# Optimization experiments

Measured on AMD Instinct MI355X. Metric: run time of the kernel, lower is better.

## Reference

```python
import jax, jax.numpy as jnp
import numpy as np

D_MODEL = 1024
NUM_HEADS = 16

def _dense_params(key, d_in, d_out):
    kw, _ = jax.random.split(key)
    # flax default: lecun_normal kernel, zeros bias
    W = jax.random.normal(kw, (d_in, d_out), dtype=jnp.float32) / np.sqrt(d_in)
    b = jnp.zeros((d_out,), dtype=jnp.float32)
    return W, b

def setup_inputs() -> dict:
    key = jax.random.key(0)
    ks = jax.random.split(key, 8)
    B, Tx, Tc = 2, 2048, 2048
    x = jax.random.normal(ks[0], (B, Tx, D_MODEL), dtype=jnp.float32)
    context = jax.random.normal(ks[1], (B, Tc, D_MODEL), dtype=jnp.float32)
    Wq, bq = _dense_params(ks[2], D_MODEL, D_MODEL)
    Wks, bks = _dense_params(ks[3], D_MODEL, D_MODEL)
    Wvs, bvs = _dense_params(ks[4], D_MODEL, D_MODEL)
    Wkc, bkc = _dense_params(ks[5], D_MODEL, D_MODEL)
    Wvc, bvc = _dense_params(ks[6], D_MODEL, D_MODEL)
    Wo, bo = _dense_params(ks[7], D_MODEL, D_MODEL)
    return {"x": x, "context": context,
            "Wq": Wq, "bq": bq, "Wks": Wks, "bks": bks, "Wvs": Wvs, "bvs": bvs,
            "Wkc": Wkc, "bkc": bkc, "Wvc": Wvc, "bvc": bvc, "Wo": Wo, "bo": bo}

def _split_heads(t, H):
    B, T, C = t.shape
    return t.reshape(B, T, H, C // H).transpose(0, 2, 1, 3)  # [B,H,T,hd]

def reference(x, context, Wq, bq, Wks, bks, Wvs, bvs, Wkc, bkc, Wvc, bvc, Wo, bo):
    H = NUM_HEADS
    head_dim = D_MODEL // H
    q = x @ Wq + bq
    k = jnp.concatenate([x @ Wks + bks, context @ Wkc + bkc], axis=1)
    v = jnp.concatenate([x @ Wvs + bvs, context @ Wvc + bvc], axis=1)
    q = _split_heads(q, H)  # [B,H,Tq,hd]
    k = _split_heads(k, H)  # [B,H,Tk,hd]
    v = _split_heads(v, H)
    attn = jnp.einsum('bhqd,bhkd->bhqk', q, k) / jnp.sqrt(jnp.float32(head_dim))
    attn = jax.nn.softmax(attn, axis=-1)
    out = jnp.einsum('bhqk,bhkd->bhqd', attn, v)
    B, _, Tq, _ = out.shape
    out = out.transpose(0, 2, 1, 3).reshape(B, Tq, D_MODEL)
    return out @ Wo + bo
```

## Files before the change

kernel.cpp:

```cpp
#include <hip/hip_runtime.h>
#include <hip/hip_bf16.h>
#include <math.h>


typedef _Float16 f16;
typedef _Float16 f16x8 __attribute__((ext_vector_type(8)));
typedef _Float16 f16x4v __attribute__((ext_vector_type(4)));
typedef _Float16 f16x2 __attribute__((ext_vector_type(2)));
typedef float    f32x4 __attribute__((ext_vector_type(4)));
typedef float    f32x16 __attribute__((ext_vector_type(16)));
typedef unsigned u32x4v __attribute__((ext_vector_type(4)));

#define MFMA_F16(a, b, c)  __builtin_amdgcn_mfma_f32_16x16x32_f16((a), (b), (c), 0, 0, 0)
#define MFMA32_F16(a, b, c) __builtin_amdgcn_mfma_f32_32x32x16_f16((a), (b), (c), 0, 0, 0)

#define QSCALE 0.18033688011112042f

__device__ __forceinline__ void glds16(const f16* g, f16* l) {
    __builtin_amdgcn_global_load_lds(
        (const __attribute__((address_space(1))) void*)g,
        (__attribute__((address_space(3))) void*)l, 16, 0, 0);
}

__device__ __forceinline__ unsigned pk16(float a, float b) {
    f16x2 t = { (f16)a, (f16)b };
    return __builtin_bit_cast(unsigned, t);
}

__global__ __launch_bounds__(256) void prep(
    const float4* __restrict__ x, const float4* __restrict__ ctx,
    f16x4v* __restrict__ xb, f16x4v* __restrict__ cb,
    const float* __restrict__ W0, const float* __restrict__ W1,
    const float* __restrict__ W2, const float* __restrict__ W3,
    const float* __restrict__ W4, const float* __restrict__ W5,
    f16* __restrict__ wt)
{
    if (blockIdx.x < 8192) {
        const int n4 = (2 * 2048 * 1024) / 4;
        int i = blockIdx.x * 256 + threadIdx.x;
        float4 v;
        f16x4v* dst;
        if (i < n4) { v = x[i];        dst = xb + i; }
        else        { v = ctx[i - n4]; dst = cb + (i - n4); }
        f16x4v h = { (f16)v.x, (f16)v.y, (f16)v.z, (f16)v.w };
        *dst = h;
        return;
    }
    const int idx = blockIdx.x - 8192;
    const int z = idx >> 10, rem = idx & 1023;
    const float* Ws[6] = { W0, W1, W2, W3, W4, W5 };
    const float* W = Ws[z];
    f16* Wt = wt + (size_t)z * (1024 * 1024);

    __shared__ float tile[32][33];
    const int tx = threadIdx.x & 31, ty = threadIdx.x >> 5;
    const int n0 = (rem & 31) * 32, k0 = (rem >> 5) * 32;

#pragma unroll
    for (int i = 0; i < 4; ++i) {
        int r = i * 8 + ty;
        tile[r][tx] = W[(size_t)(k0 + r) * 1024 + n0 + tx];
    }
    __syncthreads();
#pragma unroll
    for (int i = 0; i < 4; ++i) {
        int r = i * 8 + ty;
        Wt[(size_t)(n0 + r) * 1024 + k0 + tx] = (f16)tile[tx][r];
    }
}

#define GEMM_PROLOGUE(BN)                                                     \
    const int m0 = blockIdx.x * 128, n0 = blockIdx.y * (BN);                  \
    const int tid = threadIdx.x;                                              \
    const int w = tid >> 6, lane = tid & 63, quad = lane >> 4, l15 = lane & 15;\
    const int wm = (w >> 1) * 64, wn = (w & 1) * ((BN) / 2);                  \
    const int qsw = (quad ^ ((l15 >> 1) & 3)) * 8;                            \
    int gA[2], gB[(BN) / 64];                                                 \
    _Pragma("unroll")                                                         \
    for (int p = 0; p < 2; ++p) {                                             \
        int s = tid + p * 256;                                                \
        int r = (s >> 2) & 127, c = (s & 3) ^ ((s >> 3) & 3);                 \
        gA[p] = (m0 + r) * 1024 + c * 8;                                      \
    }                                                                         \
    _Pragma("unroll")                                                         \
    for (int p = 0; p < (BN) / 64; ++p) {                                     \
        int s = tid + p * 256;                                                \
        int r = (s >> 2) & ((BN) - 1), c = (s & 3) ^ ((s >> 3) & 3);          \
        gB[p] = (n0 + r) * 1024 + c * 8;                                      \
    }

#define GEMM_STAGE_TO(BN, buf, koff)                                          \
    _Pragma("unroll")                                                         \
    for (int p = 0; p < 2; ++p)                                               \
        glds16(&A[gA[p] + (koff)], &As[buf][(p * 256 + w * 64) * 8]);         \
    _Pragma("unroll")                                                         \
    for (int p = 0; p < (BN) / 64; ++p)                                       \
        glds16(&Bt[gB[p] + (koff)], &Bs[buf][(p * 256 + w * 64) * 8]);

__global__ __launch_bounds__(256) void proj_gemm(
    const f16* __restrict__ xb, const f16* __restrict__ cb,
    const f16* __restrict__ wt,
    const float* __restrict__ bq, const float* __restrict__ bks,
    const float* __restrict__ bkc, const float* __restrict__ bvs,
    const float* __restrict__ bvc,
    f16* __restrict__ qbuf, f16* __restrict__ kbuf, f16* __restrict__ vbuf)
{
    __shared__ alignas(16) f16 As[3][128 * 32];
    __shared__ alignas(16) f16 Bs[3][128 * 32];

    const int z = blockIdx.z;
    const f16* A = (z == 0 || z == 1 || z == 3) ? xb : cb;
    const int wslot = (z == 0) ? 0 : (z == 1) ? 1 : (z == 2) ? 3 : (z == 3) ? 2 : 4;
    const f16* Bt = wt + (size_t)wslot * 1048576;
    const float* bias = (z == 0) ? bq : (z == 1) ? bks : (z == 2) ? bkc
                        : (z == 3) ? bvs : bvc;
    const int roff = (z == 2 || z == 4) ? 2048 : 0;

    GEMM_PROLOGUE(128)
    f32x4 acc[4][4] = {};

    GEMM_STAGE_TO(128, 0, 0)
    GEMM_STAGE_TO(128, 1, 32)

    for (int it = 0; it < 32; ++it) {
        if (it < 31) { asm volatile("s_waitcnt vmcnt(4)" ::: "memory"); }
        else         { asm volatile("s_waitcnt vmcnt(0)" ::: "memory"); }
        __builtin_amdgcn_s_barrier();
        if (it + 2 < 32) {
            GEMM_STAGE_TO(128, (it + 2) % 3, (it + 2) * 32)
        }
        const f16* Asc = As[it % 3];
        const f16* Bsc = Bs[it % 3];
        f16x8 a[4], b[4];
#pragma unroll
        for (int i = 0; i < 4; ++i)
            a[i] = *(const f16x8*)&Asc[(wm + i * 16 + l15) * 32 + qsw];
#pragma unroll
        for (int i = 0; i < 4; ++i)
            b[i] = *(const f16x8*)&Bsc[(wn + i * 16 + l15) * 32 + qsw];
#pragma unroll
        for (int mi = 0; mi < 4; ++mi)
#pragma unroll
            for (int ni = 0; ni < 4; ++ni)
                acc[mi][ni] = MFMA_F16(a[mi], b[ni], acc[mi][ni]);
    }

#pragma unroll
    for (int mi = 0; mi < 4; ++mi) {
#pragma unroll
        for (int r = 0; r < 4; ++r) {
            int row = m0 + wm + mi * 16 + quad * 4 + r;
            int b_ = row >> 11, tok = row & 2047;
#pragma unroll
            for (int ni = 0; ni < 4; ++ni) {
                int col = n0 + wn + ni * 16 + l15;
                float v = acc[mi][ni][r] + bias[col];
                int bh = b_ * 16 + (col >> 6);
                int tg = roff + tok;
                if (z == 0) {
                    qbuf[((size_t)bh * 2048 + tok) * 64 + (col & 63)] = (f16)(v * QSCALE);
                } else if (z <= 2) {
                    kbuf[(size_t)bh * 262144 + (size_t)(tg >> 6) * 4096
                         + (size_t)((col >> 5) & 1) * 2048 + (tg & 63) * 32 + (col & 31)] = (f16)v;
                } else {
                    vbuf[(size_t)bh * 262144 + (size_t)tg * 64 + (col & 63)] = (f16)v;
                }
            }
        }
    }
}

__global__ __launch_bounds__(256) void transpose_v(
    const f16* __restrict__ vbuf, f16* __restrict__ vt)
{
    const int t = threadIdx.x;
    const int mt = t >> 3, md = t & 7;
    const int tok0 = blockIdx.x * 256 + mt * 8;
    const int z = blockIdx.y;
    f16x8 in[8];
#pragma unroll
    for (int i = 0; i < 8; ++i)
        in[i] = *(const f16x8*)&vbuf[((size_t)z * 4096 + tok0 + i) * 64 + md * 8];
    f16x8 ov[8];
#pragma unroll
    for (int j = 0; j < 8; ++j)
#pragma unroll
        for (int i = 0; i < 8; ++i) ov[j][i] = in[i][j];
    const int kt = tok0 >> 6, kks = (tok0 >> 5) & 1, kko = tok0 & 31;
#pragma unroll
    for (int j = 0; j < 8; ++j)
        *(f16x8*)&vt[(size_t)z * 262144 + (size_t)kt * 4096 + kks * 2048
                     + (md * 8 + j) * 32 + kko] = ov[j];
}

__global__ __launch_bounds__(256, 4) void attn_kernel(
    const f16* __restrict__ q, const f16* __restrict__ kb,
    const f16* __restrict__ vtb, f16* __restrict__ osplit,
    float* __restrict__ lsplit)
{
    __shared__ alignas(16) f16 K_lds[2][4096];
    __shared__ alignas(16) f16 V_lds[2][4096];

    const int tid = threadIdx.x;
    const int w = tid >> 6, lane = tid & 63;
    const int l31 = lane & 31, h = lane >> 5;
    const int bh = blockIdx.x, qt = blockIdx.y, sp = blockIdx.z;
    const int qbase = qt * 128;

    f16x8 qa[4];
    {
        const size_t qrow = ((size_t)bh * 2048 + qbase + w * 32 + l31) * 64;
#pragma unroll
        for (int kc = 0; kc < 4; ++kc)
            qa[kc] = *(const f16x8*)&q[qrow + kc * 16 + h * 8];
    }

    f32x16 o_acc[2] = {};
    float l_part = 0.f;

    const f16* ktile = kb + (size_t)bh * 262144 + (size_t)sp * 131072;
    const f16* vtile = vtb + (size_t)bh * 262144 + (size_t)sp * 131072;

    const int sco = ((tid >> 2) * 4 + ((tid & 3) ^ ((tid >> 3) & 3))) * 8;
    const int ksw = (l31 >> 1) & 3;
    const int wslot = w * 512;

    glds16(ktile + sco,        &K_lds[0][wslot]);
    glds16(ktile + 2048 + sco, &K_lds[0][2048 + wslot]);
    glds16(vtile + sco,        &V_lds[0][wslot]);
    glds16(vtile + 2048 + sco, &V_lds[0][2048 + wslot]);

    for (int kt = 0; kt < 32; ++kt) {
        const int cur = kt & 1;
        const f16* Kc = K_lds[cur];
        const f16* Vc = V_lds[cur];

        __syncthreads();

        if (kt != 31) {
            ktile += 4096; vtile += 4096;
            glds16(ktile + sco,        &K_lds[cur ^ 1][wslot]);
            glds16(ktile + 2048 + sco, &K_lds[cur ^ 1][2048 + wslot]);
            glds16(vtile + sco,        &V_lds[cur ^ 1][wslot]);
            glds16(vtile + 2048 + sco, &V_lds[cur ^ 1][2048 + wslot]);
        }

#pragma unroll
        for (int mt = 0; mt < 2; ++mt) {
            f32x16 s = {};
            __builtin_amdgcn_s_setprio(1);
#pragma unroll
            for (int kc = 0; kc < 4; ++kc) {
                f16x8 ka = *(const f16x8*)&Kc[(kc >> 1) * 2048
                             + (mt * 32 + l31) * 32
                             + ((((kc & 1) * 2 + h) ^ ksw)) * 8];
                s = MFMA32_F16(ka, qa[kc], s);
            }
            __builtin_amdgcn_s_setprio(0);

            float pe[16];
#pragma unroll
            for (int i = 0; i < 16; ++i) pe[i] = __builtin_amdgcn_exp2f(s[i]);

            {
                float t0 = (pe[0] + pe[1]) + (pe[2] + pe[3]);
                float t1 = (pe[4] + pe[5]) + (pe[6] + pe[7]);
                float t2 = (pe[8] + pe[9]) + (pe[10] + pe[11]);
                float t3 = (pe[12] + pe[13]) + (pe[14] + pe[15]);
                l_part += (t0 + t1) + (t2 + t3);
            }

#pragma unroll
            for (int c = 0; c < 2; ++c) {
                const int cb = c * 8;
                unsigned X0 = pk16(pe[cb + 0], pe[cb + 1]);
                unsigned X1 = pk16(pe[cb + 2], pe[cb + 3]);
                unsigned Y0 = pk16(pe[cb + 4], pe[cb + 5]);
                unsigned Y1 = pk16(pe[cb + 6], pe[cb + 7]);
                auto r0 = __builtin_amdgcn_permlane32_swap(X0, Y0, false, false);
                auto r1 = __builtin_amdgcn_permlane32_swap(X1, Y1, false, false);
                u32x4v pw;
                pw[0] = r0[0]; pw[1] = r1[0]; pw[2] = r0[1]; pw[3] = r1[1];
                f16x8 pfrag = __builtin_bit_cast(f16x8, pw);

                const int kchunk = mt * 2 + c;
                __builtin_amdgcn_s_setprio(1);
#pragma unroll
                for (int db = 0; db < 2; ++db) {
                    f16x8 va = *(const f16x8*)&Vc[(kchunk >> 1) * 2048
                                 + (db * 32 + l31) * 32
                                 + (((((kchunk & 1) * 2 + h)) ^ ksw)) * 8];
                    o_acc[db] = MFMA32_F16(va, pfrag, o_acc[db]);
                }
                __builtin_amdgcn_s_setprio(0);
            }
        }
    }

    float lf = l_part + __shfl_xor(l_part, 32, 64);
    float inv = 1.0f / lf;
    const int row = w * 32 + l31;
    const size_t sb = (size_t)(sp * 32 + bh) * 2048 + qbase;
    if (h == 0) lsplit[sb + row] = lf;
    const size_t obase = (sb + row) * 64;
#pragma unroll
    for (int db = 0; db < 2; ++db) {
#pragma unroll
        for (int g = 0; g < 4; ++g) {
            f16x4v ov;
#pragma unroll
            for (int i = 0; i < 4; ++i)
                ov[i] = (f16)(o_acc[db][g * 4 + i] * inv);
            *(f16x4v*)&osplit[obase + db * 32 + g * 8 + h * 4] = ov;
        }
    }
}

__global__ __launch_bounds__(256) void combine(
    const f16* __restrict__ osplit, const float* __restrict__ lsplit,
    f16* __restrict__ abuf)
{
    int idx = blockIdx.x * 256 + threadIdx.x;
    int d8 = idx & 7;
    int row = (idx >> 3) & 2047;
    int bh = idx >> 14;
    int b = bh >> 4, h = bh & 15;
    size_t base1 = ((size_t)bh * 2048 + row) * 64 + d8 * 8;
    size_t base2 = ((size_t)(32 + bh) * 2048 + row) * 64 + d8 * 8;
    float l1 = lsplit[bh * 2048 + row];
    float l2 = lsplit[65536 + bh * 2048 + row];
    float inv = 1.0f / (l1 + l2);
    float w1 = l1 * inv, w2 = l2 * inv;
    f16x8 a = *(const f16x8*)&osplit[base1];
    f16x8 c = *(const f16x8*)&osplit[base2];
    f16x8 out;
#pragma unroll
    for (int j = 0; j < 8; ++j)
        out[j] = (f16)(w1 * (float)a[j] + w2 * (float)c[j]);
    *(f16x8*)&abuf[((size_t)(b * 2048 + row)) * 1024 + h * 64 + d8 * 8] = out;
}

__global__ __launch_bounds__(256) void out_gemm(
    const f16* __restrict__ abuf, const f16* __restrict__ wt5,
    const float* __restrict__ bo, float* __restrict__ out)
{
    __shared__ alignas(16) f16 As[3][128 * 32];
    __shared__ alignas(16) f16 Bs[3][64 * 32];

    const f16* A = abuf;
    const f16* Bt = wt5;

    GEMM_PROLOGUE(64)
    f32x4 acc[4][2] = {};

    GEMM_STAGE_TO(64, 0, 0)
    GEMM_STAGE_TO(64, 1, 32)

    for (int it = 0; it < 32; ++it) {
        if (it < 31) { asm volatile("s_waitcnt vmcnt(3)" ::: "memory"); }
        else         { asm volatile("s_waitcnt vmcnt(0)" ::: "memory"); }
        __builtin_amdgcn_s_barrier();
        if (it + 2 < 32) {
            GEMM_STAGE_TO(64, (it + 2) % 3, (it + 2) * 32)
        }
        const f16* Asc = As[it % 3];
        const f16* Bsc = Bs[it % 3];
        f16x8 a[4], b[2];
#pragma unroll
        for (int i = 0; i < 4; ++i)
            a[i] = *(const f16x8*)&Asc[(wm + i * 16 + l15) * 32 + qsw];
#pragma unroll
        for (int i = 0; i < 2; ++i)
            b[i] = *(const f16x8*)&Bsc[(wn + i * 16 + l15) * 32 + qsw];
#pragma unroll
        for (int mi = 0; mi < 4; ++mi)
#pragma unroll
            for (int ni = 0; ni < 2; ++ni)
                acc[mi][ni] = MFMA_F16(a[mi], b[ni], acc[mi][ni]);
    }

#pragma unroll
    for (int mi = 0; mi < 4; ++mi) {
#pragma unroll
        for (int r = 0; r < 4; ++r) {
            int row = m0 + wm + mi * 16 + quad * 4 + r;
#pragma unroll
            for (int ni = 0; ni < 2; ++ni) {
                int col = n0 + wn + ni * 16 + l15;
                out[(size_t)row * 1024 + col] = acc[mi][ni][r] + bo[col];
            }
        }
    }
}

extern "C" void kernel_launch(void* const* d_in, const int* in_sizes, int n_in,
                              void* d_out, int out_size, void* d_ws, size_t ws_size,
                              hipStream_t stream)
{
    (void)in_sizes; (void)n_in; (void)out_size; (void)ws_size;

    const float* x    = (const float*)d_in[0];
    const float* ctx  = (const float*)d_in[1];
    const float* Wq   = (const float*)d_in[2];  const float* bq  = (const float*)d_in[3];
    const float* Wks  = (const float*)d_in[4];  const float* bks = (const float*)d_in[5];
    const float* Wvs  = (const float*)d_in[6];  const float* bvs = (const float*)d_in[7];
    const float* Wkc  = (const float*)d_in[8];  const float* bkc = (const float*)d_in[9];
    const float* Wvc  = (const float*)d_in[10]; const float* bvc = (const float*)d_in[11];
    const float* Wo   = (const float*)d_in[12]; const float* bo  = (const float*)d_in[13];

    char* ws = (char*)d_ws;
    f16*   xb     = (f16*)(ws + 0);
    f16*   cb     = (f16*)(ws + 8388608);
    f16*   vt     = (f16*)(ws + 0);
    f16*   wt     = (f16*)(ws + 16777216);
    float* lsplit = (float*)(ws + 16777216);
    f16*   qbuf   = (f16*)(ws + 29360128);
    f16*   kbuf   = (f16*)(ws + 37748736);
    f16*   vbuf   = (f16*)(ws + 54525952);
    f16*   osplit = (f16*)(ws + 54525952);
    f16*   abuf   = (f16*)(ws + 71303168);

    prep<<<14336, 256, 0, stream>>>((const float4*)x, (const float4*)ctx,
                                    (f16x4v*)xb, (f16x4v*)cb,
                                    Wq, Wks, Wvs, Wkc, Wvc, Wo, wt);

    proj_gemm<<<dim3(32, 8, 5), 256, 0, stream>>>(
        xb, cb, wt, bq, bks, bkc, bvs, bvc, qbuf, kbuf, vbuf);

    transpose_v<<<dim3(16, 32), 256, 0, stream>>>(vbuf, vt);

    attn_kernel<<<dim3(32, 16, 2), 256, 0, stream>>>(qbuf, kbuf, vt, osplit, lsplit);

    combine<<<2048, 256, 0, stream>>>(osplit, lsplit, abuf);

    out_gemm<<<dim3(32, 16), 256, 0, stream>>>(abuf, wt + 5 * 1048576, bo, (float*)d_out);
}
```

Baseline: 301.3 us.

## Write transposed V from projection GEMM and retile output GEMM to 64x64

The projection GEMM epilogue now writes V directly in the transposed, tiled layout that the attention kernel reads, so the separate transpose_v kernel and its extra pass over V are removed. The workspace is rearranged so osplit and vt no longer alias each other. The output GEMM moves from 128x64 to 64x64 tiles, doubling the grid to 1024 blocks for better occupancy on the many CUs, with one load per operand per stage. The cost is scattered, non-coalesced 2-byte stores in the V epilogue and less data reuse per block in the output GEMM.

```diff
diff --git a/kernel.cpp b/kernel.cpp
--- a/kernel.cpp
+++ b/kernel.cpp
@@ -103,7 +103,7 @@
     const float* __restrict__ bq, const float* __restrict__ bks,
     const float* __restrict__ bkc, const float* __restrict__ bvs,
     const float* __restrict__ bvc,
-    f16* __restrict__ qbuf, f16* __restrict__ kbuf, f16* __restrict__ vbuf)
+    f16* __restrict__ qbuf, f16* __restrict__ kbuf, f16* __restrict__ vtb)
 {
     __shared__ alignas(16) f16 As[3][128 * 32];
     __shared__ alignas(16) f16 Bs[3][128 * 32];
@@ -163,34 +163,12 @@
                     kbuf[(size_t)bh * 262144 + (size_t)(tg >> 6) * 4096
                          + (size_t)((col >> 5) & 1) * 2048 + (tg & 63) * 32 + (col & 31)] = (f16)v;
                 } else {
-                    vbuf[(size_t)bh * 262144 + (size_t)tg * 64 + (col & 63)] = (f16)v;
+                    vtb[(size_t)bh * 262144 + (size_t)(tg >> 6) * 4096
+                        + (size_t)((tg >> 5) & 1) * 2048 + (col & 63) * 32 + (tg & 31)] = (f16)v;
                 }
             }
         }
     }
-}
-
-__global__ __launch_bounds__(256) void transpose_v(
-    const f16* __restrict__ vbuf, f16* __restrict__ vt)
-{
-    const int t = threadIdx.x;
-    const int mt = t >> 3, md = t & 7;
-    const int tok0 = blockIdx.x * 256 + mt * 8;
-    const int z = blockIdx.y;
-    f16x8 in[8];
-#pragma unroll
-    for (int i = 0; i < 8; ++i)
-        in[i] = *(const f16x8*)&vbuf[((size_t)z * 4096 + tok0 + i) * 64 + md * 8];
-    f16x8 ov[8];
-#pragma unroll
-    for (int j = 0; j < 8; ++j)
-#pragma unroll
-        for (int i = 0; i < 8; ++i) ov[j][i] = in[i][j];
-    const int kt = tok0 >> 6, kks = (tok0 >> 5) & 1, kko = tok0 & 31;
-#pragma unroll
-    for (int j = 0; j < 8; ++j)
-        *(f16x8*)&vt[(size_t)z * 262144 + (size_t)kt * 4096 + kks * 2048
-                     + (md * 8 + j) * 32 + kko] = ov[j];
 }
 
 __global__ __launch_bounds__(256, 4) void attn_kernel(
@@ -344,43 +322,52 @@
     const f16* __restrict__ abuf, const f16* __restrict__ wt5,
     const float* __restrict__ bo, float* __restrict__ out)
 {
-    __shared__ alignas(16) f16 As[3][128 * 32];
+    __shared__ alignas(16) f16 As[3][64 * 32];
     __shared__ alignas(16) f16 Bs[3][64 * 32];
 
-    const f16* A = abuf;
-    const f16* Bt = wt5;
-
-    GEMM_PROLOGUE(64)
-    f32x4 acc[4][2] = {};
-
-    GEMM_STAGE_TO(64, 0, 0)
-    GEMM_STAGE_TO(64, 1, 32)
+    const int m0 = blockIdx.x * 64, n0 = blockIdx.y * 64;
+    const int tid = threadIdx.x;
+    const int w = tid >> 6, lane = tid & 63, quad = lane >> 4, l15 = lane & 15;
+    const int wm = (w >> 1) * 32, wn = (w & 1) * 32;
+    const int qsw = (quad ^ ((l15 >> 1) & 3)) * 8;
+    const int r_ = (tid >> 2) & 63, c_ = (tid & 3) ^ ((tid >> 3) & 3);
+    const int gA = (m0 + r_) * 1024 + c_ * 8;
+    const int gB = (n0 + r_) * 1024 + c_ * 8;
+
+    f32x4 acc[2][2] = {};
+
+#define OUT_STAGE(buf, koff)                                                  \
+    glds16(&abuf[gA + (koff)], &As[buf][w * 512]);                            \
+    glds16(&wt5[gB + (koff)],  &Bs[buf][w * 512]);
+
+    OUT_STAGE(0, 0)
+    OUT_STAGE(1, 32)
 
     for (int it = 0; it < 32; ++it) {
-        if (it < 31) { asm volatile("s_waitcnt vmcnt(3)" ::: "memory"); }
+        if (it < 31) { asm volatile("s_waitcnt vmcnt(2)" ::: "memory"); }
         else         { asm volatile("s_waitcnt vmcnt(0)" ::: "memory"); }
         __builtin_amdgcn_s_barrier();
         if (it + 2 < 32) {
-            GEMM_STAGE_TO(64, (it + 2) % 3, (it + 2) * 32)
+            OUT_STAGE((it + 2) % 3, (it + 2) * 32)
         }
         const f16* Asc = As[it % 3];
         const f16* Bsc = Bs[it % 3];
-        f16x8 a[4], b[2];
-#pragma unroll
-        for (int i = 0; i < 4; ++i)
+        f16x8 a[2], b[2];
+#pragma unroll
+        for (int i = 0; i < 2; ++i)
             a[i] = *(const f16x8*)&Asc[(wm + i * 16 + l15) * 32 + qsw];
 #pragma unroll
         for (int i = 0; i < 2; ++i)
             b[i] = *(const f16x8*)&Bsc[(wn + i * 16 + l15) * 32 + qsw];
 #pragma unroll
-        for (int mi = 0; mi < 4; ++mi)
+        for (int mi = 0; mi < 2; ++mi)
 #pragma unroll
             for (int ni = 0; ni < 2; ++ni)
                 acc[mi][ni] = MFMA_F16(a[mi], b[ni], acc[mi][ni]);
     }
 
 #pragma unroll
-    for (int mi = 0; mi < 4; ++mi) {
+    for (int mi = 0; mi < 2; ++mi) {
 #pragma unroll
         for (int r = 0; r < 4; ++r) {
             int row = m0 + wm + mi * 16 + quad * 4 + r;
@@ -411,13 +398,12 @@
     char* ws = (char*)d_ws;
     f16*   xb     = (f16*)(ws + 0);
     f16*   cb     = (f16*)(ws + 8388608);
-    f16*   vt     = (f16*)(ws + 0);
+    f16*   osplit = (f16*)(ws + 0);
     f16*   wt     = (f16*)(ws + 16777216);
     float* lsplit = (float*)(ws + 16777216);
     f16*   qbuf   = (f16*)(ws + 29360128);
     f16*   kbuf   = (f16*)(ws + 37748736);
-    f16*   vbuf   = (f16*)(ws + 54525952);
-    f16*   osplit = (f16*)(ws + 54525952);
+    f16*   vt     = (f16*)(ws + 54525952);
     f16*   abuf   = (f16*)(ws + 71303168);
 
     prep<<<14336, 256, 0, stream>>>((const float4*)x, (const float4*)ctx,
@@ -425,13 +411,11 @@
                                     Wq, Wks, Wvs, Wkc, Wvc, Wo, wt);
 
     proj_gemm<<<dim3(32, 8, 5), 256, 0, stream>>>(
-        xb, cb, wt, bq, bks, bkc, bvs, bvc, qbuf, kbuf, vbuf);
-
-    transpose_v<<<dim3(16, 32), 256, 0, stream>>>(vbuf, vt);
+        xb, cb, wt, bq, bks, bkc, bvs, bvc, qbuf, kbuf, vt);
 
     attn_kernel<<<dim3(32, 16, 2), 256, 0, stream>>>(qbuf, kbuf, vt, osplit, lsplit);
 
     combine<<<2048, 256, 0, stream>>>(osplit, lsplit, abuf);
 
-    out_gemm<<<dim3(32, 16), 256, 0, stream>>>(abuf, wt + 5 * 1048576, bo, (float*)d_out);
-}
+    out_gemm<<<dim3(64, 16), 256, 0, stream>>>(abuf, wt + 5 * 1048576, bo, (float*)d_out);
+}
```

New measurement: 310.4 us. 1.03x slower.

## Fuse split-KV combine into output projection GEMM A-tile loading

Applied to the files above, without the earlier changes.

Removes the separate combine kernel and instead merges the two split-KV attention partial outputs inside out_gemm while staging the A tile into shared memory. The output GEMM tile shrinks from 128x64 to 64x64 and the grid doubles, with register-prefetched A loads and a double-buffered A tile. This removes the abuf write and re-read plus one launch. In exchange, each N-column block recomputes the merge (16x redundant reads of osplit), and the smaller tile lowers per-block MFMA reuse.

```diff
diff --git a/kernel.cpp b/kernel.cpp
--- a/kernel.cpp
+++ b/kernel.cpp
@@ -316,71 +316,88 @@
     }
 }
 
-__global__ __launch_bounds__(256) void combine(
+__global__ __launch_bounds__(256) void out_gemm(
     const f16* __restrict__ osplit, const float* __restrict__ lsplit,
-    f16* __restrict__ abuf)
-{
-    int idx = blockIdx.x * 256 + threadIdx.x;
-    int d8 = idx & 7;
-    int row = (idx >> 3) & 2047;
-    int bh = idx >> 14;
-    int b = bh >> 4, h = bh & 15;
-    size_t base1 = ((size_t)bh * 2048 + row) * 64 + d8 * 8;
-    size_t base2 = ((size_t)(32 + bh) * 2048 + row) * 64 + d8 * 8;
-    float l1 = lsplit[bh * 2048 + row];
-    float l2 = lsplit[65536 + bh * 2048 + row];
-    float inv = 1.0f / (l1 + l2);
-    float w1 = l1 * inv, w2 = l2 * inv;
-    f16x8 a = *(const f16x8*)&osplit[base1];
-    f16x8 c = *(const f16x8*)&osplit[base2];
-    f16x8 out;
-#pragma unroll
-    for (int j = 0; j < 8; ++j)
-        out[j] = (f16)(w1 * (float)a[j] + w2 * (float)c[j]);
-    *(f16x8*)&abuf[((size_t)(b * 2048 + row)) * 1024 + h * 64 + d8 * 8] = out;
-}
-
-__global__ __launch_bounds__(256) void out_gemm(
-    const f16* __restrict__ abuf, const f16* __restrict__ wt5,
-    const float* __restrict__ bo, float* __restrict__ out)
-{
-    __shared__ alignas(16) f16 As[3][128 * 32];
+    const f16* __restrict__ wt5, const float* __restrict__ bo,
+    float* __restrict__ out)
+{
+    __shared__ alignas(16) f16 As[2][64 * 32];
     __shared__ alignas(16) f16 Bs[3][64 * 32];
 
-    const f16* A = abuf;
-    const f16* Bt = wt5;
-
-    GEMM_PROLOGUE(64)
-    f32x4 acc[4][2] = {};
-
-    GEMM_STAGE_TO(64, 0, 0)
-    GEMM_STAGE_TO(64, 1, 32)
+    const int m0 = blockIdx.x * 64, n0 = blockIdx.y * 64;
+    const int tid = threadIdx.x;
+    const int w = tid >> 6, lane = tid & 63, quad = lane >> 4, l15 = lane & 15;
+    const int wm = (w >> 1) * 32, wn = (w & 1) * 32;
+    const int qsw = (quad ^ ((l15 >> 1) & 3)) * 8;
+    const int r_ = (tid >> 2) & 63, c_ = (tid & 3) ^ ((tid >> 3) & 3);
+    const int rowg = m0 + r_;
+    const int b_ = rowg >> 11, tok = rowg & 2047;
+    const int gB = (n0 + r_) * 1024 + c_ * 8;
+    const int lslot = w * 512 + lane * 8;
+
+    f32x4 acc[2][2] = {};
+
+#define OA(s, it) (&osplit[(((size_t)(s) * 32 + b_ * 16 + ((it) >> 1)) * 2048 \
+                            + tok) * 64 + ((it) & 1) * 32 + c_ * 8])
+#define OL(s, it) ((s) * 65536 + (b_ * 16 + ((it) >> 1)) * 2048 + tok)
+
+#define MERGE_WRITE(buf, a1, a2, l1, l2)                                      \
+    {                                                                         \
+        float inv_ = 1.0f / ((l1) + (l2));                                    \
+        float w1_ = (l1) * inv_, w2_ = (l2) * inv_;                           \
+        f16x8 m_;                                                             \
+        _Pragma("unroll")                                                     \
+        for (int j_ = 0; j_ < 8; ++j_)                                        \
+            m_[j_] = (f16)(w1_ * (float)(a1)[j_] + w2_ * (float)(a2)[j_]);    \
+        *(f16x8*)&As[buf][lslot] = m_;                                        \
+    }
+
+    glds16(&wt5[gB], &Bs[0][w * 512]);
+    f16x8 a1 = *(const f16x8*)OA(0, 0);
+    f16x8 a2 = *(const f16x8*)OA(1, 0);
+    float l1 = lsplit[OL(0, 0)];
+    float l2 = lsplit[OL(1, 0)];
+    glds16(&wt5[gB + 32], &Bs[1][w * 512]);
+    MERGE_WRITE(0, a1, a2, l1, l2)
+    asm volatile("s_waitcnt lgkmcnt(0)" ::: "memory");
+    __builtin_amdgcn_s_barrier();
 
     for (int it = 0; it < 32; ++it) {
-        if (it < 31) { asm volatile("s_waitcnt vmcnt(3)" ::: "memory"); }
-        else         { asm volatile("s_waitcnt vmcnt(0)" ::: "memory"); }
-        __builtin_amdgcn_s_barrier();
-        if (it + 2 < 32) {
-            GEMM_STAGE_TO(64, (it + 2) % 3, (it + 2) * 32)
-        }
-        const f16* Asc = As[it % 3];
+        f16x8 na1, na2;
+        float nl1, nl2;
+        if (it < 31) {
+            na1 = *(const f16x8*)OA(0, it + 1);
+            na2 = *(const f16x8*)OA(1, it + 1);
+            nl1 = lsplit[OL(0, it + 1)];
+            nl2 = lsplit[OL(1, it + 1)];
+            if (it + 2 < 32)
+                glds16(&wt5[gB + (it + 2) * 32], &Bs[(it + 2) % 3][w * 512]);
+        }
+
+        const f16* Asc = As[it & 1];
         const f16* Bsc = Bs[it % 3];
-        f16x8 a[4], b[2];
-#pragma unroll
-        for (int i = 0; i < 4; ++i)
+        f16x8 a[2], b[2];
+#pragma unroll
+        for (int i = 0; i < 2; ++i)
             a[i] = *(const f16x8*)&Asc[(wm + i * 16 + l15) * 32 + qsw];
 #pragma unroll
         for (int i = 0; i < 2; ++i)
             b[i] = *(const f16x8*)&Bsc[(wn + i * 16 + l15) * 32 + qsw];
 #pragma unroll
-        for (int mi = 0; mi < 4; ++mi)
+        for (int mi = 0; mi < 2; ++mi)
 #pragma unroll
             for (int ni = 0; ni < 2; ++ni)
                 acc[mi][ni] = MFMA_F16(a[mi], b[ni], acc[mi][ni]);
-    }
-
-#pragma unroll
-    for (int mi = 0; mi < 4; ++mi) {
+
+        if (it < 31) {
+            MERGE_WRITE((it + 1) & 1, na1, na2, nl1, nl2)
+        }
+        asm volatile("s_waitcnt lgkmcnt(0)" ::: "memory");
+        __builtin_amdgcn_s_barrier();
+    }
+
+#pragma unroll
+    for (int mi = 0; mi < 2; ++mi) {
 #pragma unroll
         for (int r = 0; r < 4; ++r) {
             int row = m0 + wm + mi * 16 + quad * 4 + r;
@@ -391,6 +408,9 @@
             }
         }
     }
+#undef OA
+#undef OL
+#undef MERGE_WRITE
 }
 
 extern "C" void kernel_launch(void* const* d_in, const int* in_sizes, int n_in,
@@ -418,7 +438,6 @@
     f16*   kbuf   = (f16*)(ws + 37748736);
     f16*   vbuf   = (f16*)(ws + 54525952);
     f16*   osplit = (f16*)(ws + 54525952);
-    f16*   abuf   = (f16*)(ws + 71303168);
 
     prep<<<14336, 256, 0, stream>>>((const float4*)x, (const float4*)ctx,
                                     (f16x4v*)xb, (f16x4v*)cb,
@@ -431,7 +450,6 @@
 
     attn_kernel<<<dim3(32, 16, 2), 256, 0, stream>>>(qbuf, kbuf, vt, osplit, lsplit);
 
-    combine<<<2048, 256, 0, stream>>>(osplit, lsplit, abuf);
-
-    out_gemm<<<dim3(32, 16), 256, 0, stream>>>(abuf, wt + 5 * 1048576, bo, (float*)d_out);
-}
+    out_gemm<<<dim3(64, 16), 256, 0, stream>>>(osplit, lsplit,
+                                               wt + 5 * 1048576, bo, (float*)d_out);
+}
```

Measured after the change: 307.4 us. 2.0% more time.
